# Performance work log

Measured on AMD Instinct MI355X. Metric: run time of the kernel, lower is better.

The kernel has to match this reference:

```python
import jax, jax.numpy as jnp
import numpy as np

B, K, C, Q, NCLS = 16, 36, 2048, 1024, 16
LIN = 1024
DIN = 2 * C + 16 + Q  # 5136


def _linear_params(key, din, dout, scale=0.02):
    kw, kb = jax.random.split(key)
    W = jax.random.normal(kw, (din, dout), dtype=jnp.float32) * scale
    b = jax.random.normal(kb, (dout,), dtype=jnp.float32) * scale
    return W, b


def setup_inputs() -> dict:
    key = jax.random.key(0)
    ks = jax.random.split(key, 12)
    box_feats = jax.random.normal(ks[0], (B, K, C), dtype=jnp.float32)
    q_feats = jax.random.normal(ks[1], (B, Q), dtype=jnp.float32)
    # valid boxes: x2>x1, y2>y1 so areas are strictly positive (no div-by-zero)
    x1y1 = jax.random.uniform(ks[2], (B, K, 2), dtype=jnp.float32)
    wh = jax.random.uniform(ks[3], (B, K, 2), dtype=jnp.float32, minval=0.05, maxval=1.0)
    box_coords = jnp.concatenate([x1y1, x1y1 + wh, wh], axis=-1)  # [B,K,6]
    index = jax.random.randint(ks[4], (B,), 1, K + 1)  # ragged box counts in [1,K]
    wholefeat = jax.random.normal(ks[5], (B, C), dtype=jnp.float32)
    pooled = jax.random.normal(ks[6], (B, C), dtype=jnp.float32)
    W1, b1 = _linear_params(ks[7], DIN, LIN)
    W2, b2 = _linear_params(ks[8], LIN, LIN)
    W3, b3 = _linear_params(ks[9], LIN, LIN)
    Wf1, bf1 = _linear_params(ks[10], LIN, LIN // 2)
    Wf2, bf2 = _linear_params(ks[11], LIN // 2, NCLS)
    return {"wholefeat": wholefeat, "pooled": pooled, "box_feats": box_feats,
            "q_feats": q_feats, "box_coords": box_coords, "index": index,
            "W1": W1, "b1": b1, "W2": W2, "b2": b2, "W3": W3, "b3": b3,
            "Wf1": Wf1, "bf1": bf1, "Wf2": Wf2, "bf2": bf2}


def _rn_forward(box_feats, q_feats, box_coords, index,
                W1, b1, W2, b2, W3, b3, Wf1, bf1, Wf2, bf2):
    b_, k_, c_ = box_feats.shape
    # ragged -> padded + mask: pair (i,j) valid iff i < index[b] and j < index[b]
    valid = (jnp.arange(k_)[None, :] < index[:, None]).astype(box_feats.dtype)  # [B,K]
    pair_mask = valid[:, :, None] * valid[:, None, :]  # [B,K,K]

    # pairwise dot of region features
    dot = jnp.einsum('bid,bjd->bij', box_feats, box_feats)[..., None]  # [B,K,K,1]

    bc = box_coords  # [B,K,6]
    area = (bc[..., 2] - bc[..., 0]) * (bc[..., 3] - bc[..., 1])  # [B,K]
    lr = jnp.maximum(0.0, jnp.minimum(bc[:, :, None, 2], bc[:, None, :, 2])
                     - jnp.maximum(bc[:, :, None, 0], bc[:, None, :, 0]))
    ud = jnp.maximum(0.0, jnp.minimum(bc[:, :, None, 3], bc[:, None, :, 3])
                     - jnp.maximum(bc[:, :, None, 1], bc[:, None, :, 1]))
    overlap = lr * ud  # [B,K,K]
    area_i = area[:, :, None]
    area_j = area[:, None, :]
    iou = (overlap / (area_i + area_j - overlap))[..., None]
    o_ij = (overlap / area_i)[..., None]
    o_ji = (overlap / area_j)[..., None]

    b_ij = jnp.broadcast_to(bc[:, :, None, :], (b_, k_, k_, 6))
    b_ji = jnp.broadcast_to(bc[:, None, :, :], (b_, k_, k_, 6))
    o_i = jnp.broadcast_to(box_feats[:, :, None, :], (b_, k_, k_, c_))
    o_j = jnp.broadcast_to(box_feats[:, None, :, :], (b_, k_, k_, c_))
    qst = jnp.broadcast_to(q_feats[:, None, None, :], (b_, k_, k_, q_feats.shape[-1]))

    # [B,K,K,5136] = [o_i, o_j, qst, dot, b_ij, b_ji, iou, o_ij, o_ji]
    feat = jnp.concatenate([o_i, o_j, qst, dot, b_ij, b_ji, iou, o_ij, o_ji], axis=-1)

    h = jax.nn.relu(feat @ W1 + b1)
    h = jax.nn.relu(h @ W2 + b2)
    h = jax.nn.relu(h @ W3 + b3)  # [B,K,K,1024]

    # masked sum-pool over all valid (i,j) pairs
    g = jnp.einsum('bijh,bij->bh', h, pair_mask)  # [B,1024]

    out = jax.nn.relu(g @ Wf1 + bf1) @ Wf2 + bf2  # [B,Ncls]
    return out


def reference(wholefeat, pooled, box_feats, q_feats, box_coords, index,
              W1, b1, W2, b2, W3, b3, Wf1, bf1, Wf2, bf2):
    # wholefeat / pooled are unused by the original forward as well
    return _rn_forward(box_feats, q_feats, box_coords, index,
                       W1, b1, W2, b2, W3, b3, Wf1, bf1, Wf2, bf2)
```

## Files before the change

### kernel.cpp

```cpp
#include <hip/hip_runtime.h>
#include <stdint.h>

typedef unsigned short u16;
typedef __attribute__((ext_vector_type(8))) short short8;
typedef __attribute__((ext_vector_type(4))) float f32x4;

#define Bn 16
#define Kn 36
#define Cn 2048
#define Qn 1024
#define LINn 1024
#define NPp 1296
#define NPAIRn 20736
#define NBIn 576

__device__ __forceinline__ u16 f2bf(float f) {
  union { float f; unsigned int u; } v; v.f = f;
  unsigned int r = v.u + 0x7FFFu + ((v.u >> 16) & 1u);
  return (u16)(r >> 16);
}

__device__ __forceinline__ void llds16(const void* g, void* l) {
  __builtin_amdgcn_global_load_lds((const __attribute__((address_space(1))) void*)g,
                                   (__attribute__((address_space(3))) void*)l, 16, 0, 0);
}

__global__ void k_transpose_all(const float* __restrict__ W1, const float* __restrict__ W2,
                                const float* __restrict__ W3, u16* __restrict__ W1abT,
                                u16* __restrict__ W2T, u16* __restrict__ W3T) {
  __shared__ float tile[32][33];
  int z = blockIdx.z;
  const float* src; u16* dst; int ld_dst;
  if (z == 0)      { if (blockIdx.y >= 32) return; src = W2; dst = W2T; ld_dst = 1024; }
  else if (z == 1) { if (blockIdx.y >= 32) return; src = W3; dst = W3T; ld_dst = 1024; }
  else if (z == 2) { src = W1; dst = W1abT; ld_dst = 2048; }
  else             { src = W1 + (size_t)2048 * 1024; dst = W1abT + (size_t)1024 * 2048; ld_dst = 2048; }
  int n0 = blockIdx.x * 32, k0 = blockIdx.y * 32;
  int tx = threadIdx.x & 31, ty = threadIdx.x >> 5;
#pragma unroll
  for (int r = 0; r < 32; r += 8)
    tile[ty + r][tx] = src[(size_t)(k0 + ty + r) * 1024 + (n0 + tx)];
  __syncthreads();
#pragma unroll
  for (int r = 0; r < 32; r += 8)
    dst[(size_t)(n0 + ty + r) * ld_dst + (k0 + tx)] = f2bf(tile[tx][ty + r]);
}

__global__ void k_f2b(const float4* __restrict__ src, ushort4* __restrict__ dst, int n4) {
  int i = blockIdx.x * 256 + threadIdx.x;
  if (i < n4) {
    float4 v = src[i];
    ushort4 o;
    o.x = f2bf(v.x); o.y = f2bf(v.y); o.z = f2bf(v.z); o.w = f2bf(v.w);
    dst[i] = o;
  }
}

__global__ void k_build(const int* __restrict__ index, int* __restrict__ pairList,
                        int* __restrict__ batchC, int* __restrict__ cnt2) {
  __shared__ int offs[17];
  int tid = threadIdx.x;
  int b = blockIdx.x;
  if (tid == 0) {
    int o = 0;
    for (int i = 0; i < Bn; ++i) { offs[i] = o; int v = index[i]; o += v * v; }
    offs[16] = o;
    if (b == 0) {
      cnt2[0] = o;
      cnt2[1] = (o + 127) & ~127;
    }
  }
  __syncthreads();
  int v = index[b]; int n = v * v; int base = offs[b];
  for (int t = tid; t < n; t += 256) {
    int i = t / v, j = t - i * v;
    pairList[base + t] = b * NPp + i * Kn + j;
    batchC[base + t] = b;
  }
  if (b == 0) {
    int total = offs[16];
    int totalPad = (total + 127) & ~127;
    for (int t = total + tid; t < totalPad; t += 256) {
      pairList[t] = 0;
      batchC[t] = 0;
    }
  }
}

__global__ void k_pcinit(const float* __restrict__ b1, float* __restrict__ Pc) {
  int n = blockIdx.x * 256 + threadIdx.x;
  float v = b1[n];
#pragma unroll
  for (int b = 0; b < Bn; ++b) Pc[b * LINn + n] = v;
}

__global__ void k_pconst(const float* __restrict__ q, const float* __restrict__ W1,
                         float* __restrict__ Pc) {
  __shared__ float qs[Bn][32];
  int n = blockIdx.x * 256 + threadIdx.x;
  int k0 = blockIdx.y * 32;
  const float* Wq = W1 + (size_t)(2 * Cn) * LINn;
  for (int t = threadIdx.x; t < Bn * 32; t += 256) {
    int b = t >> 5, k = t & 31;
    qs[b][k] = q[b * Qn + k0 + k];
  }
  __syncthreads();
  float acc[Bn];
#pragma unroll
  for (int b = 0; b < Bn; ++b) acc[b] = 0.f;
  for (int k = 0; k < 32; ++k) {
    float w = Wq[(size_t)(k0 + k) * LINn + n];
#pragma unroll
    for (int b = 0; b < Bn; ++b) acc[b] += qs[b][k] * w;
  }
#pragma unroll
  for (int b = 0; b < Bn; ++b) atomicAdd(&Pc[b * LINn + n], acc[b]);
}

__global__ void k_pairscalars(const float* __restrict__ bfm, const float* __restrict__ bc,
                              const int* __restrict__ pairList, const int* __restrict__ cnt2,
                              float* __restrict__ dotC, float* __restrict__ iouC,
                              float* __restrict__ oijC, float* __restrict__ ojiC) {
  int cnt = cnt2[0];
  int lane = threadIdx.x & 63;
  for (int m = blockIdx.x * 4 + (threadIdx.x >> 6); m < cnt; m += gridDim.x * 4) {
    int p = pairList[m];
    int b = p / NPp, rem = p - b * NPp, i = rem / Kn, j = rem - (rem / Kn) * Kn;
    const float4* Ai = (const float4*)(bfm + (size_t)(b * Kn + i) * Cn);
    const float4* Aj = (const float4*)(bfm + (size_t)(b * Kn + j) * Cn);
    float s = 0.f;
#pragma unroll
    for (int t = 0; t < Cn / 4 / 64; ++t) {
      float4 x = Ai[lane + t * 64], y = Aj[lane + t * 64];
      s += x.x * y.x + x.y * y.y + x.z * y.z + x.w * y.w;
    }
#pragma unroll
    for (int o = 32; o > 0; o >>= 1) s += __shfl_down(s, o);
    if (lane == 0) {
      const float* ci = bc + (size_t)(b * Kn + i) * 6;
      const float* cj = bc + (size_t)(b * Kn + j) * 6;
      float ai = (ci[2] - ci[0]) * (ci[3] - ci[1]);
      float aj = (cj[2] - cj[0]) * (cj[3] - cj[1]);
      float lr = fmaxf(0.f, fminf(ci[2], cj[2]) - fmaxf(ci[0], cj[0]));
      float ud = fmaxf(0.f, fminf(ci[3], cj[3]) - fmaxf(ci[1], cj[1]));
      float ov = lr * ud;
      dotC[m] = s;
      iouC[m] = ov / (ai + aj - ov);
      oijC[m] = ov / ai;
      ojiC[m] = ov / aj;
    }
  }
}

__global__ void k_pinit(const float* __restrict__ Pc, const float* __restrict__ bc,
                        const float* __restrict__ W1, float* __restrict__ P12) {
  int bi = blockIdx.x;
  int b = bi / Kn;
  const float* c = bc + (size_t)bi * 6;
  const float* W = W1 + (size_t)(2 * Cn + Qn + 1) * LINn;
#pragma unroll
  for (int it = 0; it < 8; ++it) {
    int cc = it * 256 + threadIdx.x;
    int n = cc & 1023;
    int rbase = (cc < 1024) ? 0 : 6;
    float a = 0.f;
#pragma unroll
    for (int t = 0; t < 6; ++t) a += c[t] * W[(size_t)(rbase + t) * LINn + n];
    if (cc < 1024) a += Pc[b * LINn + n];
    P12[(size_t)bi * 2048 + cc] = a;
  }
}

__global__ void k_h1(const float* __restrict__ P12,
                     const float* __restrict__ dotC, const float* __restrict__ iouC,
                     const float* __restrict__ oijC, const float* __restrict__ ojiC,
                     const int* __restrict__ pairList, const int* __restrict__ cnt2,
                     const float* __restrict__ W1, u16* __restrict__ H1) {
  int cnt = cnt2[0];
  int t = threadIdx.x;
  const float4* wd = (const float4*)(W1 + (size_t)(2 * Cn + Qn) * LINn);
  const float4* wu = (const float4*)(W1 + (size_t)(2 * Cn + Qn + 13) * LINn);
  const float4* wa = (const float4*)(W1 + (size_t)(2 * Cn + Qn + 14) * LINn);
  const float4* wb = (const float4*)(W1 + (size_t)(2 * Cn + Qn + 15) * LINn);
  float4 e1 = wd[t], e2 = wu[t], e3 = wa[t], e4 = wb[t];
  for (int m = blockIdx.x; m < cnt; m += gridDim.x) {
    int p = pairList[m];
    int b = p / NPp, rem = p - b * NPp, i = rem / Kn, j = rem - (rem / Kn) * Kn;
    float d = dotC[m], u = iouC[m], o1 = oijC[m], o2 = ojiC[m];
    const float4* p1 = (const float4*)(P12 + (size_t)(b * Kn + i) * 2048);
    const float4* p2 = (const float4*)(P12 + (size_t)(b * Kn + j) * 2048 + 1024);
    ushort4* outp = (ushort4*)(H1 + (size_t)m * 1024);
    float4 v1 = p1[t], v2 = p2[t];
    ushort4 o;
    o.x = f2bf(fmaxf(v1.x + v2.x + d * e1.x + u * e2.x + o1 * e3.x + o2 * e4.x, 0.f));
    o.y = f2bf(fmaxf(v1.y + v2.y + d * e1.y + u * e2.y + o1 * e3.y + o2 * e4.y, 0.f));
    o.z = f2bf(fmaxf(v1.z + v2.z + d * e1.z + u * e2.z + o1 * e3.z + o2 * e4.z, 0.f));
    o.w = f2bf(fmaxf(v1.w + v2.w + d * e1.w + u * e2.w + o1 * e3.w + o2 * e4.w, 0.f));
    outp[t] = o;
  }
}

template <int EPI>
__global__ void __launch_bounds__(256) k_gemm(
    const u16* __restrict__ A, const u16* __restrict__ BT,
    int N, int K, int KC, int Mvalid, const int* __restrict__ cnt2,
    float* __restrict__ Cf, u16* __restrict__ Cb,
    const float* __restrict__ bias,
    const int* __restrict__ batchC, float* __restrict__ G) {
  __shared__ u16 Alds[2][128 * 64];
  __shared__ u16 Blds[2][64 * 64];
  __shared__ float Gpart[(EPI == 2) ? (Bn * 64) : 4];

  const int tid = threadIdx.x;
  const int wave = tid >> 6, lane = tid & 63;
  const int wm = (wave >> 1) * 64, wn = (wave & 1) * 32;

  int Mv = Mvalid;
  int m0, n0;
  if (EPI == 0) {
    m0 = blockIdx.x * 128;
    n0 = blockIdx.y * 64;
  } else {
    Mv = cnt2[0];
    int nMt = (Mv + 127) >> 7;
    int nact = nMt * 16;
    int id = blockIdx.x;
    if (id >= nact) return;
    int q = nact >> 3, r = nact & 7;
    int xcd = id & 7, rank = id >> 3;
    int wg = (xcd < r ? xcd * (q + 1) : r * (q + 1) + (xcd - r) * q) + rank;
    m0 = (wg >> 4) * 128;
    n0 = (wg & 15) * 64;
  }
  if (EPI == 2) {
    for (int t = tid; t < Bn * 64; t += 256) Gpart[t] = 0.f;
  }

  f32x4 zero = {0.f, 0.f, 0.f, 0.f};
  f32x4 acc[4][2];
#pragma unroll
  for (int x = 0; x < 4; ++x)
#pragma unroll
    for (int y = 0; y < 2; ++y) acc[x][y] = zero;

  const int srow = tid >> 3;
  const int sslot = ((tid & 7) ^ (srow & 7)) * 16;
  const size_t ldb = (size_t)K * 2;

  auto stage = [&](int buf, int k0) {
    char* aB = (char*)Alds[buf] + wave * 1024;
    char* bB = (char*)Blds[buf] + wave * 1024;
#pragma unroll
    for (int c = 0; c < 4; ++c) {
      int rg = m0 + c * 32 + srow; if (rg >= Mv) rg = Mv - 1;
      llds16((const char*)A + (size_t)rg * ldb + (size_t)k0 * 2 + sslot, aB + c * 4096);
    }
#pragma unroll
    for (int c = 0; c < 2; ++c) {
      int rg = n0 + c * 32 + srow;
      llds16((const char*)BT + (size_t)rg * ldb + (size_t)k0 * 2 + sslot, bB + c * 4096);
    }
  };

  auto compute = [&](int buf) {
    const char* Ab = (const char*)Alds[buf];
    const char* Bb = (const char*)Blds[buf];
    short8 af[2][4], bfr[2][2];
#pragma unroll
    for (int kk = 0; kk < 2; ++kk) {
#pragma unroll
      for (int f = 0; f < 4; ++f) {
        int rA = wm + f * 16 + (lane & 15);
        int sl = ((kk * 4 + (lane >> 4)) ^ (rA & 7)) * 16;
        af[kk][f] = *(const short8*)(Ab + (size_t)rA * 128 + sl);
      }
#pragma unroll
      for (int f = 0; f < 2; ++f) {
        int rB = wn + f * 16 + (lane & 15);
        int sl = ((kk * 4 + (lane >> 4)) ^ (rB & 7)) * 16;
        bfr[kk][f] = *(const short8*)(Bb + (size_t)rB * 128 + sl);
      }
    }
#pragma unroll
    for (int kk = 0; kk < 2; ++kk)
#pragma unroll
      for (int x = 0; x < 4; ++x)
#pragma unroll
        for (int y = 0; y < 2; ++y)
          acc[x][y] = __builtin_amdgcn_mfma_f32_16x16x32_bf16(af[kk][x], bfr[kk][y],
                                                              acc[x][y], 0, 0, 0);
  };

  const int kbeg = blockIdx.z * KC;
  const int nt = KC >> 6;
  stage(0, kbeg);
  for (int t = 0; t < nt; ++t) {
    if (t + 1 < nt) {
      stage((t + 1) & 1, kbeg + (t + 1) * 64);
      asm volatile("s_waitcnt vmcnt(6)" ::: "memory");
    } else {
      asm volatile("s_waitcnt vmcnt(0)" ::: "memory");
    }
    __builtin_amdgcn_s_barrier();
    compute(t & 1);
    __builtin_amdgcn_s_barrier();
  }

  if (EPI == 0) {
#pragma unroll
    for (int x = 0; x < 4; ++x) {
      int rb = m0 + wm + x * 16 + (lane >> 4) * 4;
#pragma unroll
      for (int r = 0; r < 4; ++r) {
        int row = rb + r;
        if (row < Mv) {
#pragma unroll
          for (int y = 0; y < 2; ++y)
            atomicAdd(&Cf[(size_t)row * N + (n0 + wn + y * 16 + (lane & 15))],
                      acc[x][y][r]);
        }
      }
    }
  } else if (EPI == 1) {
#pragma unroll
    for (int x = 0; x < 4; ++x) {
      int rb = m0 + wm + x * 16 + (lane >> 4) * 4;
#pragma unroll
      for (int r = 0; r < 4; ++r) {
        int row = rb + r;
#pragma unroll
        for (int y = 0; y < 2; ++y) {
          int col = n0 + wn + y * 16 + (lane & 15);
          Cb[(size_t)row * N + col] = f2bf(fmaxf(acc[x][y][r] + bias[col], 0.f));
        }
      }
    }
  } else {
    const int cnt = Mv;
#pragma unroll
    for (int x = 0; x < 4; ++x) {
      int rb = m0 + wm + x * 16 + (lane >> 4) * 4;
      int b0 = batchC[rb], b1 = batchC[rb + 1], b2 = batchC[rb + 2], b3 = batchC[rb + 3];
      float mk0 = (rb     < cnt) ? 1.f : 0.f;
      float mk1 = (rb + 1 < cnt) ? 1.f : 0.f;
      float mk2 = (rb + 2 < cnt) ? 1.f : 0.f;
      float mk3 = (rb + 3 < cnt) ? 1.f : 0.f;
#pragma unroll
      for (int y = 0; y < 2; ++y) {
        int coll = wn + y * 16 + (lane & 15);
        float bs = bias[n0 + coll];
        float s0 = mk0 * fmaxf(acc[x][y][0] + bs, 0.f);
        float s1 = mk1 * fmaxf(acc[x][y][1] + bs, 0.f);
        float s2 = mk2 * fmaxf(acc[x][y][2] + bs, 0.f);
        float s3 = mk3 * fmaxf(acc[x][y][3] + bs, 0.f);
        if (b0 == b3) {
          atomicAdd(&Gpart[b0 * 64 + coll], s0 + s1 + s2 + s3);
        } else {
          atomicAdd(&Gpart[b0 * 64 + coll], s0);
          atomicAdd(&Gpart[b1 * 64 + coll], s1);
          atomicAdd(&Gpart[b2 * 64 + coll], s2);
          atomicAdd(&Gpart[b3 * 64 + coll], s3);
        }
      }
    }
    __syncthreads();
    for (int t2 = tid; t2 < Bn * 64; t2 += 256) {
      float v = Gpart[t2];
      if (v != 0.f) atomicAdd(&G[(t2 >> 6) * LINn + n0 + (t2 & 63)], v);
    }
  }
}

__global__ void k_final1(const float* __restrict__ G, const float* __restrict__ Wf1,
                         float* __restrict__ S) {
  __shared__ float g[128];
  int b = blockIdx.x, kz = blockIdx.y, tid = threadIdx.x;
  if (tid < 128) g[tid] = G[b * 1024 + kz * 128 + tid];
  __syncthreads();
  float acc = 0.f;
  const float* W = Wf1 + (size_t)(kz * 128) * 512 + tid;
  for (int k = 0; k < 128; ++k) acc += g[k] * W[(size_t)k * 512];
  atomicAdd(&S[b * 512 + tid], acc);
}

__global__ void k_final2(const float* __restrict__ S, const float* __restrict__ bf1,
                         const float* __restrict__ Wf2, const float* __restrict__ bf2,
                         float* __restrict__ out) {
  __shared__ float mid[512];
  __shared__ float part[256];
  int b = blockIdx.x, tid = threadIdx.x;
  for (int t = tid; t < 512; t += 256) mid[t] = fmaxf(S[b * 512 + t] + bf1[t], 0.f);
  __syncthreads();
  int o = tid & 15, seg = tid >> 4;
  float s = 0.f;
#pragma unroll
  for (int t = 0; t < 32; ++t) {
    int j = seg * 32 + t;
    s += mid[j] * Wf2[j * 16 + o];
  }
  part[tid] = s;
  __syncthreads();
  if (tid < 16) {
    float v = bf2[tid];
#pragma unroll
    for (int sg = 0; sg < 16; ++sg) v += part[sg * 16 + tid];
    out[b * 16 + tid] = v;
  }
}

extern "C" void kernel_launch(void* const* d_in, const int* in_sizes, int n_in,
                              void* d_out, int out_size, void* d_ws, size_t ws_size,
                              hipStream_t stream) {
  const float* box_feats  = (const float*)d_in[2];
  const float* q_feats    = (const float*)d_in[3];
  const float* box_coords = (const float*)d_in[4];
  const int*   index      = (const int*)d_in[5];
  const float* W1  = (const float*)d_in[6];
  const float* b1  = (const float*)d_in[7];
  const float* W2  = (const float*)d_in[8];
  const float* b2  = (const float*)d_in[9];
  const float* W3  = (const float*)d_in[10];
  const float* b3  = (const float*)d_in[11];
  const float* Wf1 = (const float*)d_in[12];
  const float* bf1 = (const float*)d_in[13];
  const float* Wf2 = (const float*)d_in[14];
  const float* bf2 = (const float*)d_in[15];
  float* out = (float*)d_out;

  char* ws = (char*)d_ws;
  size_t off = 0;
  auto alloc = [&](size_t bytes) { void* p = ws + off; off += (bytes + 255) & ~(size_t)255; return p; };
  u16* W1abT = (u16*)alloc((size_t)2048 * 2048 * 2);
  u16* W2T   = (u16*)alloc((size_t)1024 * 1024 * 2);
  u16* W3T   = (u16*)alloc((size_t)1024 * 1024 * 2);
  u16* BFb   = (u16*)alloc((size_t)NBIn * Cn * 2);
  float* P12  = (float*)alloc((size_t)640 * 2048 * 4);
  float* Pc   = (float*)alloc((size_t)Bn * LINn * 4);
  float* dotC = (float*)alloc((size_t)NPAIRn * 4);
  float* iouC = (float*)alloc((size_t)NPAIRn * 4);
  float* oijC = (float*)alloc((size_t)NPAIRn * 4);
  float* ojiC = (float*)alloc((size_t)NPAIRn * 4);
  int* pairList = (int*)alloc((size_t)NPAIRn * 4);
  int* batchC   = (int*)alloc((size_t)NPAIRn * 4);
  int* cnt2     = (int*)alloc(64);
  float* G  = (float*)alloc((size_t)Bn * LINn * 4);
  float* S  = (float*)alloc((size_t)Bn * 512 * 4);
  u16* H1 = (u16*)alloc((size_t)NPAIRn * 1024 * 2);
  u16* H2 = (u16*)alloc((size_t)NPAIRn * 1024 * 2);

  k_transpose_all<<<dim3(32, 64, 4), 256, 0, stream>>>(W1, W2, W3, W1abT, W2T, W3T);
  k_f2b<<<(NBIn * Cn / 4 + 255) / 256, 256, 0, stream>>>((const float4*)box_feats,
                                                         (ushort4*)BFb, NBIn * Cn / 4);
  k_build<<<16, 256, 0, stream>>>(index, pairList, batchC, cnt2);
  hipMemsetAsync(G, 0, (size_t)Bn * LINn * 4, stream);
  hipMemsetAsync(S, 0, (size_t)Bn * 512 * 4, stream);
  k_pcinit<<<4, 256, 0, stream>>>(b1, Pc);
  k_pconst<<<dim3(4, 32), 256, 0, stream>>>(q_feats, W1, Pc);
  k_pairscalars<<<648, 256, 0, stream>>>(box_feats, box_coords, pairList, cnt2,
                                         dotC, iouC, oijC, ojiC);
  k_pinit<<<NBIn, 256, 0, stream>>>(Pc, box_coords, W1, P12);
  k_gemm<0><<<dim3(5, 32, 4), 256, 0, stream>>>(BFb, W1abT, 2048, 2048, 512, NBIn, nullptr,
                                                P12, nullptr, nullptr, nullptr, nullptr);
  k_h1<<<2592, 256, 0, stream>>>(P12, dotC, iouC, oijC, ojiC, pairList, cnt2, W1, H1);
  k_gemm<1><<<dim3(2592, 1, 1), 256, 0, stream>>>(H1, W2T, 1024, 1024, 1024, 0, cnt2,
                                                  nullptr, H2, b2, nullptr, nullptr);
  k_gemm<2><<<dim3(2592, 1, 1), 256, 0, stream>>>(H2, W3T, 1024, 1024, 1024, 0, cnt2,
                                                  nullptr, nullptr, b3, batchC, G);
  k_final1<<<dim3(16, 8), 512, 0, stream>>>(G, Wf1, S);
  k_final2<<<16, 256, 0, stream>>>(S, bf1, Wf2, bf2, out);
}
```

Before: 156.8 us.

## Retile MLP layer-2/3 GEMMs to 256x256 tiles with 512-thread blocks

New measurement: 172.1 us. 9.8% more time.

```diff
diff --git a/kernel.cpp b/kernel.cpp
--- a/kernel.cpp
+++ b/kernel.cpp
@@ -79,7 +79,7 @@
   }
   if (b == 0) {
     int total = offs[16];
-    int totalPad = (total + 127) & ~127;
+    int totalPad = (total + 255) & ~255;
     for (int t = total + tid; t < totalPad; t += 256) {
       pairList[t] = 0;
       batchC[t] = 0;
@@ -200,41 +200,18 @@
   }
 }
 
-template <int EPI>
-__global__ void __launch_bounds__(256) k_gemm(
+__global__ void __launch_bounds__(256) k_gemmP(
     const u16* __restrict__ A, const u16* __restrict__ BT,
-    int N, int K, int KC, int Mvalid, const int* __restrict__ cnt2,
-    float* __restrict__ Cf, u16* __restrict__ Cb,
-    const float* __restrict__ bias,
-    const int* __restrict__ batchC, float* __restrict__ G) {
+    int N, int K, int KC, int Mvalid,
+    float* __restrict__ Cf) {
   __shared__ u16 Alds[2][128 * 64];
   __shared__ u16 Blds[2][64 * 64];
-  __shared__ float Gpart[(EPI == 2) ? (Bn * 64) : 4];
-
   const int tid = threadIdx.x;
   const int wave = tid >> 6, lane = tid & 63;
   const int wm = (wave >> 1) * 64, wn = (wave & 1) * 32;
-
-  int Mv = Mvalid;
-  int m0, n0;
-  if (EPI == 0) {
-    m0 = blockIdx.x * 128;
-    n0 = blockIdx.y * 64;
-  } else {
-    Mv = cnt2[0];
-    int nMt = (Mv + 127) >> 7;
-    int nact = nMt * 16;
-    int id = blockIdx.x;
-    if (id >= nact) return;
-    int q = nact >> 3, r = nact & 7;
-    int xcd = id & 7, rank = id >> 3;
-    int wg = (xcd < r ? xcd * (q + 1) : r * (q + 1) + (xcd - r) * q) + rank;
-    m0 = (wg >> 4) * 128;
-    n0 = (wg & 15) * 64;
-  }
-  if (EPI == 2) {
-    for (int t = tid; t < Bn * 64; t += 256) Gpart[t] = 0.f;
-  }
+  const int m0 = blockIdx.x * 128;
+  const int n0 = blockIdx.y * 64;
+  const int Mv = Mvalid;
 
   f32x4 zero = {0.f, 0.f, 0.f, 0.f};
   f32x4 acc[4][2];
@@ -306,47 +283,146 @@
     __builtin_amdgcn_s_barrier();
   }
 
-  if (EPI == 0) {
-#pragma unroll
-    for (int x = 0; x < 4; ++x) {
+#pragma unroll
+  for (int x = 0; x < 4; ++x) {
+    int rb = m0 + wm + x * 16 + (lane >> 4) * 4;
+#pragma unroll
+    for (int r = 0; r < 4; ++r) {
+      int row = rb + r;
+      if (row < Mv) {
+#pragma unroll
+        for (int y = 0; y < 2; ++y)
+          atomicAdd(&Cf[(size_t)row * N + (n0 + wn + y * 16 + (lane & 15))],
+                    acc[x][y][r]);
+      }
+    }
+  }
+}
+
+template <int EPI>
+__global__ void __launch_bounds__(512, 2) k_gemm2(
+    const u16* __restrict__ A, const u16* __restrict__ BT,
+    const int* __restrict__ cnt2,
+    u16* __restrict__ Cb, const float* __restrict__ bias,
+    const int* __restrict__ batchC, float* __restrict__ G) {
+  __shared__ u16 Alds[2][256 * 64];
+  __shared__ u16 Blds[2][256 * 64];
+
+  const int tid = threadIdx.x;
+  const int wave = tid >> 6, lane = tid & 63;
+  const int wm = (wave >> 2) * 128;
+  const int wn = (wave & 3) * 64;
+
+  const int cnt = cnt2[0];
+  const int nMt = (cnt + 255) >> 8;
+  const int nact = nMt * 4;
+  int id = blockIdx.x;
+  if (id >= nact) return;
+  int q = nact >> 3, r = nact & 7;
+  int xcd = id & 7, rank = id >> 3;
+  int wg = (xcd < r ? xcd * (q + 1) : r * (q + 1) + (xcd - r) * q) + rank;
+  const int m0 = (wg >> 2) * 256;
+  const int n0 = (wg & 3) * 256;
+
+  f32x4 zero = {0.f, 0.f, 0.f, 0.f};
+  f32x4 acc[8][4];
+#pragma unroll
+  for (int x = 0; x < 8; ++x)
+#pragma unroll
+    for (int y = 0; y < 4; ++y) acc[x][y] = zero;
+
+  const int srow = tid >> 3;
+  const int sslot = ((tid & 7) ^ (srow & 7)) * 16;
+  const size_t ldb = (size_t)1024 * 2;
+
+  auto stage = [&](int buf, int k0) {
+    char* aB = (char*)Alds[buf] + srow * 128 + (tid & 7) * 16;
+    char* bB = (char*)Blds[buf] + srow * 128 + (tid & 7) * 16;
+#pragma unroll
+    for (int c = 0; c < 4; ++c) {
+      int rg = m0 + c * 64 + srow; if (rg >= cnt) rg = cnt - 1;
+      llds16((const char*)A + (size_t)rg * ldb + (size_t)k0 * 2 + sslot, aB + c * 8192);
+    }
+#pragma unroll
+    for (int c = 0; c < 4; ++c) {
+      int rg = n0 + c * 64 + srow;
+      llds16((const char*)BT + (size_t)rg * ldb + (size_t)k0 * 2 + sslot, bB + c * 8192);
+    }
+  };
+
+  auto compute = [&](int buf) {
+    const char* Ab = (const char*)Alds[buf];
+    const char* Bb = (const char*)Blds[buf];
+#pragma unroll
+    for (int kk = 0; kk < 2; ++kk) {
+      short8 af[8], bfr[4];
+#pragma unroll
+      for (int f = 0; f < 8; ++f) {
+        int rA = wm + f * 16 + (lane & 15);
+        int sl = ((kk * 4 + (lane >> 4)) ^ (rA & 7)) * 16;
+        af[f] = *(const short8*)(Ab + (size_t)rA * 128 + sl);
+      }
+#pragma unroll
+      for (int f = 0; f < 4; ++f) {
+        int rB = wn + f * 16 + (lane & 15);
+        int sl = ((kk * 4 + (lane >> 4)) ^ (rB & 7)) * 16;
+        bfr[f] = *(const short8*)(Bb + (size_t)rB * 128 + sl);
+      }
+#pragma unroll
+      for (int x = 0; x < 8; ++x)
+#pragma unroll
+        for (int y = 0; y < 4; ++y)
+          acc[x][y] = __builtin_amdgcn_mfma_f32_16x16x32_bf16(af[x], bfr[y],
+                                                              acc[x][y], 0, 0, 0);
+    }
+  };
+
+  const int nt = 16;
+  stage(0, 0);
+  for (int t = 0; t < nt; ++t) {
+    if (t + 1 < nt) {
+      stage((t + 1) & 1, (t + 1) * 64);
+      asm volatile("s_waitcnt vmcnt(8)" ::: "memory");
+    } else {
+      asm volatile("s_waitcnt vmcnt(0)" ::: "memory");
+    }
+    __builtin_amdgcn_s_barrier();
+    compute(t & 1);
+    __builtin_amdgcn_s_barrier();
+  }
+
+  if (EPI == 1) {
+#pragma unroll
+    for (int x = 0; x < 8; ++x) {
       int rb = m0 + wm + x * 16 + (lane >> 4) * 4;
 #pragma unroll
       for (int r = 0; r < 4; ++r) {
         int row = rb + r;
-        if (row < Mv) {
-#pragma unroll
-          for (int y = 0; y < 2; ++y)
-            atomicAdd(&Cf[(size_t)row * N + (n0 + wn + y * 16 + (lane & 15))],
-                      acc[x][y][r]);
+#pragma unroll
+        for (int y = 0; y < 4; ++y) {
+          int col = n0 + wn + y * 16 + (lane & 15);
+          Cb[(size_t)row * 1024 + col] = f2bf(fmaxf(acc[x][y][r] + bias[col], 0.f));
         }
       }
     }
-  } else if (EPI == 1) {
-#pragma unroll
-    for (int x = 0; x < 4; ++x) {
+  } else {
+    float* Gpart = (float*)&Alds[0][0];
+    for (int t2 = tid; t2 < Bn * 256; t2 += 512) Gpart[t2] = 0.f;
+    __syncthreads();
+#pragma unroll
+    for (int x = 0; x < 8; ++x) {
       int rb = m0 + wm + x * 16 + (lane >> 4) * 4;
-#pragma unroll
-      for (int r = 0; r < 4; ++r) {
-        int row = rb + r;
-#pragma unroll
-        for (int y = 0; y < 2; ++y) {
-          int col = n0 + wn + y * 16 + (lane & 15);
-          Cb[(size_t)row * N + col] = f2bf(fmaxf(acc[x][y][r] + bias[col], 0.f));
-        }
-      }
-    }
-  } else {
-    const int cnt = Mv;
-#pragma unroll
-    for (int x = 0; x < 4; ++x) {
-      int rb = m0 + wm + x * 16 + (lane >> 4) * 4;
-      int b0 = batchC[rb], b1 = batchC[rb + 1], b2 = batchC[rb + 2], b3 = batchC[rb + 3];
+      int rc0 = (rb     < cnt) ? rb     : (cnt - 1);
+      int rc1 = (rb + 1 < cnt) ? rb + 1 : (cnt - 1);
+      int rc2 = (rb + 2 < cnt) ? rb + 2 : (cnt - 1);
+      int rc3 = (rb + 3 < cnt) ? rb + 3 : (cnt - 1);
+      int b0 = batchC[rc0], b1 = batchC[rc1], b2 = batchC[rc2], b3 = batchC[rc3];
       float mk0 = (rb     < cnt) ? 1.f : 0.f;
       float mk1 = (rb + 1 < cnt) ? 1.f : 0.f;
       float mk2 = (rb + 2 < cnt) ? 1.f : 0.f;
       float mk3 = (rb + 3 < cnt) ? 1.f : 0.f;
 #pragma unroll
-      for (int y = 0; y < 2; ++y) {
+      for (int y = 0; y < 4; ++y) {
         int coll = wn + y * 16 + (lane & 15);
         float bs = bias[n0 + coll];
         float s0 = mk0 * fmaxf(acc[x][y][0] + bs, 0.f);
@@ -354,19 +430,19 @@
         float s2 = mk2 * fmaxf(acc[x][y][2] + bs, 0.f);
         float s3 = mk3 * fmaxf(acc[x][y][3] + bs, 0.f);
         if (b0 == b3) {
-          atomicAdd(&Gpart[b0 * 64 + coll], s0 + s1 + s2 + s3);
+          atomicAdd(&Gpart[b0 * 256 + coll], s0 + s1 + s2 + s3);
         } else {
-          atomicAdd(&Gpart[b0 * 64 + coll], s0);
-          atomicAdd(&Gpart[b1 * 64 + coll], s1);
-          atomicAdd(&Gpart[b2 * 64 + coll], s2);
-          atomicAdd(&Gpart[b3 * 64 + coll], s3);
+          atomicAdd(&Gpart[b0 * 256 + coll], s0);
+          atomicAdd(&Gpart[b1 * 256 + coll], s1);
+          atomicAdd(&Gpart[b2 * 256 + coll], s2);
+          atomicAdd(&Gpart[b3 * 256 + coll], s3);
         }
       }
     }
     __syncthreads();
-    for (int t2 = tid; t2 < Bn * 64; t2 += 256) {
+    for (int t2 = tid; t2 < Bn * 256; t2 += 512) {
       float v = Gpart[t2];
-      if (v != 0.f) atomicAdd(&G[(t2 >> 6) * LINn + n0 + (t2 & 63)], v);
+      if (v != 0.f) atomicAdd(&G[(t2 >> 8) * LINn + n0 + (t2 & 255)], v);
     }
   }
 }
@@ -440,13 +516,13 @@
   float* iouC = (float*)alloc((size_t)NPAIRn * 4);
   float* oijC = (float*)alloc((size_t)NPAIRn * 4);
   float* ojiC = (float*)alloc((size_t)NPAIRn * 4);
-  int* pairList = (int*)alloc((size_t)NPAIRn * 4);
-  int* batchC   = (int*)alloc((size_t)NPAIRn * 4);
+  int* pairList = (int*)alloc((size_t)(NPAIRn + 256) * 4);
+  int* batchC   = (int*)alloc((size_t)(NPAIRn + 256) * 4);
   int* cnt2     = (int*)alloc(64);
   float* G  = (float*)alloc((size_t)Bn * LINn * 4);
   float* S  = (float*)alloc((size_t)Bn * 512 * 4);
-  u16* H1 = (u16*)alloc((size_t)NPAIRn * 1024 * 2);
-  u16* H2 = (u16*)alloc((size_t)NPAIRn * 1024 * 2);
+  u16* H1 = (u16*)alloc((size_t)(NPAIRn + 256) * 1024 * 2);
+  u16* H2 = (u16*)alloc((size_t)(NPAIRn + 256) * 1024 * 2);
 
   k_transpose_all<<<dim3(32, 64, 4), 256, 0, stream>>>(W1, W2, W3, W1abT, W2T, W3T);
   k_f2b<<<(NBIn * Cn / 4 + 255) / 256, 256, 0, stream>>>((const float4*)box_feats,
@@ -459,13 +535,10 @@
   k_pairscalars<<<648, 256, 0, stream>>>(box_feats, box_coords, pairList, cnt2,
                                          dotC, iouC, oijC, ojiC);
   k_pinit<<<NBIn, 256, 0, stream>>>(Pc, box_coords, W1, P12);
-  k_gemm<0><<<dim3(5, 32, 4), 256, 0, stream>>>(BFb, W1abT, 2048, 2048, 512, NBIn, nullptr,
-                                                P12, nullptr, nullptr, nullptr, nullptr);
+  k_gemmP<<<dim3(5, 32, 4), 256, 0, stream>>>(BFb, W1abT, 2048, 2048, 512, NBIn, P12);
   k_h1<<<2592, 256, 0, stream>>>(P12, dotC, iouC, oijC, ojiC, pairList, cnt2, W1, H1);
-  k_gemm<1><<<dim3(2592, 1, 1), 256, 0, stream>>>(H1, W2T, 1024, 1024, 1024, 0, cnt2,
-                                                  nullptr, H2, b2, nullptr, nullptr);
-  k_gemm<2><<<dim3(2592, 1, 1), 256, 0, stream>>>(H2, W3T, 1024, 1024, 1024, 0, cnt2,
-                                                  nullptr, nullptr, b3, batchC, G);
+  k_gemm2<1><<<dim3(324, 1, 1), 512, 0, stream>>>(H1, W2T, cnt2, H2, b2, nullptr, nullptr);
+  k_gemm2<2><<<dim3(324, 1, 1), 512, 0, stream>>>(H2, W3T, cnt2, nullptr, b3, batchC, G);
   k_final1<<<dim3(16, 8), 512, 0, stream>>>(G, Wf1, S);
   k_final2<<<16, 256, 0, stream>>>(S, bf1, Wf2, bf2, out);
 }
```
